# Optimization experiments

Hardware: AMD Instinct MI355X
Metric: run time of the kernel (lower is better)

## Reference

```python
import jax, jax.numpy as jnp
import numpy as np

N_EMBD = 1024  # C in forward; scale is C**-0.5 (full embed dim, per source)


def setup_inputs() -> dict:
    key = jax.random.key(0)
    k1, k2, k3, k4 = jax.random.split(key, 4)
    B, T, C, H = 4, 4096, N_EMBD, 64
    x = jax.random.normal(k1, (B, T, C), dtype=jnp.float32)
    # weights stored as [in, out] = [n_embd, head_size]
    Wq = jax.random.normal(k2, (C, H), dtype=jnp.float32) * (C ** -0.5)
    Wk = jax.random.normal(k3, (C, H), dtype=jnp.float32) * (C ** -0.5)
    Wv = jax.random.normal(k4, (C, H), dtype=jnp.float32) * (C ** -0.5)
    return {"x": x, "Wq": Wq, "Wk": Wk, "Wv": Wv}


def reference(x, Wq, Wk, Wv):
    # x: [B, T, C]; projections to head_size H
    C = x.shape[-1]
    q = jnp.einsum('btc,ch->bth', x, Wq)  # [B,T,H]
    k = jnp.einsum('btc,ch->bth', x, Wk)  # [B,T,H]
    v = jnp.einsum('btc,ch->bth', x, Wv)  # [B,T,H]
    # scores scaled by C**-0.5 (full embed dim, matching original module)
    wei = jnp.einsum('bth,bsh->bts', q, k) * (C ** -0.5)  # [B,T,T]
    wei = jax.nn.softmax(wei, axis=-1)  # dropout p=0 -> identity
    out = jnp.einsum('bts,bsh->bth', wei, v)  # [B,T,H]
    return out
```

## Files before the change

kernel.cpp:

```cpp
#include <hip/hip_runtime.h>
#include <hip/hip_bf16.h>


#define BB 4
#define TT 4096
#define CC 1024
#define HH 64

typedef __attribute__((ext_vector_type(8))) short bf16x8;
typedef __attribute__((ext_vector_type(4))) float f32x4;

#if __has_builtin(__builtin_amdgcn_exp2f)
#define EXP2(x) __builtin_amdgcn_exp2f(x)
#else
#define EXP2(x) exp2f(x)
#endif

__device__ __forceinline__ short f2bf(float f) {
  union { float f; unsigned u; } v; v.f = f;
  unsigned r = v.u + 0x7fffu + ((v.u >> 16) & 1u);
  return (short)(r >> 16);
}

__device__ __forceinline__ unsigned pk2bf(float lo, float hi) {
  __hip_bfloat162 p = __float22bfloat162_rn(make_float2(lo, hi));
  return *reinterpret_cast<unsigned*>(&p);
}

__device__ __forceinline__ void gload16(const void* g, short* l) {
  __builtin_amdgcn_global_load_lds(
      (const __attribute__((address_space(1))) void*)g,
      (__attribute__((address_space(3))) void*)l, 16, 0, 0);
}

#define WAITVM0() asm volatile("s_waitcnt vmcnt(0)" ::: "memory")

__global__ void wtf_kernel(const float* __restrict__ Wq, const float* __restrict__ Wk,
                           const float* __restrict__ Wv, short* __restrict__ WtF) {
  int idx = blockIdx.x * 256 + threadIdx.x;
  int lane = idx & 63, ks = (idx >> 6) & 31, nf = idx >> 11;
  int l15 = lane & 15, lg = lane >> 4;
  int n = nf * 16 + l15;
  const float* W = (n < HH) ? Wq : ((n < 2 * HH) ? Wk : Wv);
  float sc = (n < HH) ? (0.03125f * 1.44269504f) : 1.0f;
  int k0 = ks * 32 + lg * 8, h = n & (HH - 1);
  bf16x8 r;
#pragma unroll
  for (int j = 0; j < 8; ++j) r[j] = f2bf(W[(k0 + j) * HH + h] * sc);
  *(bf16x8*)(WtF + (size_t)idx * 8) = r;
}

__launch_bounds__(256, 2)
__global__ void projX_kernel(const float* __restrict__ x, const short* __restrict__ WtF,
                             short* __restrict__ qo, short* __restrict__ kFo,
                             short* __restrict__ vFo) {
  __shared__ __align__(16) short xs[32768];
  int t = threadIdx.x;
  int row0 = blockIdx.x * 16;
  int wave = t >> 6, lane = t & 63;
  int l15 = lane & 15, lg = lane >> 4;

  {
    const float* xb = x + (size_t)row0 * CC;
    int lp = lane ^ (lane >> 3);
#pragma unroll
    for (int k2 = 0; k2 < 16; ++k2) {
      int ks = wave * 8 + (k2 >> 1);
      int ln = (k2 & 1) * 32 + (lp >> 1);
      int h  = lp & 1;
      const float* src = xb + (size_t)(ln & 15) * CC + ks * 32 + (ln >> 4) * 8 + h * 4;
      short* dst = xs + ((size_t)wave * 1024 + (size_t)k2 * 64) * 8;
      gload16(src, dst);
    }
  }

  int nf0 = wave * 3;
  const short* wp = WtF + ((size_t)nf0 * 32 * 64 + (size_t)lane) * 8;

  f32x4 acc[3];
#pragma unroll
  for (int j = 0; j < 3; ++j) acc[j] = (f32x4){0.f, 0.f, 0.f, 0.f};

  WAITVM0();
  __syncthreads();

  const char* xsb = (const char*)xs;
  int m = (lane >> 2) & 7;
  int roA = ((lane * 2) ^ m) * 16;
  int roB = ((lane * 2 + 1) ^ m) * 16;

#define LDA(KS, AV)                                                  \
  {                                                                  \
    float4 fa_ = *(const float4*)(xsb + (KS) * 2048 + roA);          \
    float4 fb_ = *(const float4*)(xsb + (KS) * 2048 + roB);          \
    unsigned* au_ = (unsigned*)&(AV);                                \
    au_[0] = pk2bf(fa_.x, fa_.y); au_[1] = pk2bf(fa_.z, fa_.w);      \
    au_[2] = pk2bf(fb_.x, fb_.y); au_[3] = pk2bf(fb_.z, fb_.w);      \
  }

  bf16x8 wA[3], wB[3];
#pragma unroll
  for (int j = 0; j < 3; ++j) wA[j] = *(const bf16x8*)(wp + (size_t)j * 32 * 512);

#pragma unroll
  for (int ks = 0; ks < 32; ks += 2) {
#pragma unroll
    for (int j = 0; j < 3; ++j)
      wB[j] = *(const bf16x8*)(wp + ((size_t)j * 32 + ks + 1) * 512);
    bf16x8 a0;
    LDA(ks, a0)
#pragma unroll
    for (int j = 0; j < 3; ++j)
      acc[j] = __builtin_amdgcn_mfma_f32_16x16x32_bf16(a0, wA[j], acc[j], 0, 0, 0);
    if (ks + 2 < 32) {
#pragma unroll
      for (int j = 0; j < 3; ++j)
        wA[j] = *(const bf16x8*)(wp + ((size_t)j * 32 + ks + 2) * 512);
    }
    bf16x8 a1;
    LDA(ks + 1, a1)
#pragma unroll
    for (int j = 0; j < 3; ++j)
      acc[j] = __builtin_amdgcn_mfma_f32_16x16x32_bf16(a1, wB[j], acc[j], 0, 0, 0);
  }
#undef LDA

  int b  = row0 >> 12;
  int kt = (row0 & 4095) >> 6;
  int cf = (row0 >> 4) & 3;
  short* ksl = xs;
  short* vsl = xs + 1152;

  __syncthreads();

#pragma unroll
  for (int j = 0; j < 3; ++j) {
    int nf = nf0 + j;
    int h = (nf & 3) * 16 + l15;
    if (nf < 4) {
#pragma unroll
      for (int reg = 0; reg < 4; ++reg)
        qo[(size_t)(row0 + lg * 4 + reg) * HH + h] = f2bf(acc[j][reg]);
    } else if (nf < 8) {
#pragma unroll
      for (int reg = 0; reg < 4; ++reg)
        ksl[(lg * 4 + reg) * 72 + h] = f2bf(acc[j][reg]);
    } else {
      uint2 w2;
      w2.x = pk2bf(acc[j][0], acc[j][1]);
      w2.y = pk2bf(acc[j][2], acc[j][3]);
      *(uint2*)(vsl + h * 24 + lg * 4) = w2;
    }
  }
  __syncthreads();

  size_t tileoff = ((size_t)b * 64 + kt) * 4096;
  if (t < 128) {
    int ks2 = t >> 6, ln = t & 63;
    int l15o = ln & 15, lgo = ln >> 4;
    bf16x8 r = *(const bf16x8*)(ksl + l15o * 72 + ks2 * 32 + lgo * 8);
    *(bf16x8*)(kFo + tileoff + (size_t)(cf * 2 + ks2) * 512 + ln * 8) = r;
  } else if (t < 256) {
    int t2 = t - 128;
    int hf = t2 >> 5, lgl = (t2 >> 4) & 1, l15o = t2 & 15;
    bf16x8 r = *(const bf16x8*)(vsl + (hf * 16 + l15o) * 24 + lgl * 8);
    int lnout = (2 * (cf & 1) + lgl) * 16 + l15o;
    *(bf16x8*)(vFo + tileoff + (size_t)(hf * 2 + (cf >> 1)) * 512 + lnout * 8) = r;
  }
}

__launch_bounds__(512, 4)
__global__ void attnW_kernel(const short* __restrict__ q, const short* __restrict__ kF,
                             const short* __restrict__ vF, float* __restrict__ out) {
  __shared__ __align__(16) short ps[8][2560];
  __shared__ __align__(16) float macc[32][68];
  __shared__ float lL[32];
  int wave = threadIdx.x >> 6, lane = threadIdx.x & 63;
  int l15 = lane & 15, lg = lane >> 4;
  int low3 = blockIdx.x & 7;
  int b  = low3 >> 1;
  int qt = ((blockIdx.x >> 3) << 1) | (low3 & 1);
  int brow0 = qt * 32;

  const short* qb = q + ((size_t)b * TT + brow0 + l15) * HH;
  bf16x8 qa[2][2];
#pragma unroll
  for (int g = 0; g < 2; ++g) {
    qa[g][0] = *(const bf16x8*)(qb + g * 16 * HH + lg * 8);
    qa[g][1] = *(const bf16x8*)(qb + g * 16 * HH + 32 + lg * 8);
  }

  bf16x8 ones;
#pragma unroll
  for (int j = 0; j < 8; ++j) ones[j] = (short)0x3F80;

  const short* kfb = kF + (size_t)b * 262144 + (size_t)lane * 8;
  const short* vfb = vF + (size_t)b * 262144 + (size_t)lane * 8;

  f32x4 acc[2][4], accl[2];
#pragma unroll
  for (int g = 0; g < 2; ++g) {
#pragma unroll
    for (int i = 0; i < 4; ++i) acc[g][i] = (f32x4){0.f, 0.f, 0.f, 0.f};
    accl[g] = (f32x4){0.f, 0.f, 0.f, 0.f};
  }

  char* psw = (char*)&ps[wave][0];
  int xorv = (l15 >> 3) << 4;
  int pwbase = l15 * 80;
  int pr = l15 * 80 + ((lg << 4) ^ xorv);

  for (int t = wave * 16; t < wave * 16 + 16; ++t) {
    const short* kp = kfb + (size_t)t * 2048;
    const short* vp = vfb + (size_t)(t >> 1) * 4096 + (size_t)(t & 1) * 512;
    bf16x8 kf[4], vf[4];
#pragma unroll
    for (int ld = 0; ld < 4; ++ld) kf[ld] = *(const bf16x8*)(kp + ld * 512);
#pragma unroll
    for (int hf = 0; hf < 4; ++hf) vf[hf] = *(const bf16x8*)(vp + hf * 1024);
#pragma unroll
    for (int g = 0; g < 2; ++g)
#pragma unroll
      for (int cf = 0; cf < 2; ++cf) {
        f32x4 t4 = (f32x4){0.f, 0.f, 0.f, 0.f};
        t4 = __builtin_amdgcn_mfma_f32_16x16x32_bf16(kf[cf * 2], qa[g][0], t4, 0, 0, 0);
        t4 = __builtin_amdgcn_mfma_f32_16x16x32_bf16(kf[cf * 2 + 1], qa[g][1], t4, 0, 0, 0);
        float p0 = EXP2(t4[0]), p1 = EXP2(t4[1]);
        float p2 = EXP2(t4[2]), p3 = EXP2(t4[3]);
        unsigned w01 = pk2bf(p0, p1);
        unsigned w23 = pk2bf(p2, p3);
        int cb = (cf << 5) + (lg << 3);
        *(unsigned*)(psw + g * 1280 + pwbase + ((cb) ^ xorv)) = w01;
        *(unsigned*)(psw + g * 1280 + pwbase + ((cb + 4) ^ xorv)) = w23;
      }
    bf16x8 pa0 = *(const bf16x8*)(psw + pr);
    bf16x8 pa1 = *(const bf16x8*)(psw + 1280 + pr);
    __builtin_amdgcn_s_setprio(1);
#pragma unroll
    for (int hf = 0; hf < 4; ++hf) {
      acc[0][hf] = __builtin_amdgcn_mfma_f32_16x16x32_bf16(pa0, vf[hf], acc[0][hf], 0, 0, 0);
      acc[1][hf] = __builtin_amdgcn_mfma_f32_16x16x32_bf16(pa1, vf[hf], acc[1][hf], 0, 0, 0);
    }
    accl[0] = __builtin_amdgcn_mfma_f32_16x16x32_bf16(pa0, ones, accl[0], 0, 0, 0);
    accl[1] = __builtin_amdgcn_mfma_f32_16x16x32_bf16(pa1, ones, accl[1], 0, 0, 0);
    __builtin_amdgcn_s_setprio(0);
  }

#pragma unroll
  for (int ph = 0; ph < 8; ++ph) {
    if (wave == ph) {
#pragma unroll
      for (int g = 0; g < 2; ++g)
#pragma unroll
        for (int reg = 0; reg < 4; ++reg) {
          int row = g * 16 + lg * 4 + reg;
          if (ph == 0) {
#pragma unroll
            for (int hf = 0; hf < 4; ++hf)
              macc[row][hf * 16 + l15] = acc[g][hf][reg];
            if (l15 == 0) lL[row] = accl[g][reg];
          } else {
#pragma unroll
            for (int hf = 0; hf < 4; ++hf)
              macc[row][hf * 16 + l15] += acc[g][hf][reg];
            if (l15 == 0) lL[row] += accl[g][reg];
          }
        }
    }
    __syncthreads();
  }

  {
    int tt = threadIdx.x;
    int r = tt >> 4, c0 = (tt & 15) * 4;
    float linv = 1.0f / lL[r];
    float4 o;
    o.x = macc[r][c0 + 0] * linv; o.y = macc[r][c0 + 1] * linv;
    o.z = macc[r][c0 + 2] * linv; o.w = macc[r][c0 + 3] * linv;
    *(float4*)(out + ((size_t)b * TT + brow0 + r) * HH + c0) = o;
  }
}

extern "C" void kernel_launch(void* const* d_in, const int* in_sizes, int n_in,
                              void* d_out, int out_size, void* d_ws, size_t ws_size,
                              hipStream_t stream) {
  const float* x  = (const float*)d_in[0];
  const float* Wq = (const float*)d_in[1];
  const float* Wk = (const float*)d_in[2];
  const float* Wv = (const float*)d_in[3];
  float* out = (float*)d_out;

  char* ws = (char*)d_ws;
  short* WtF = (short*)ws;
  short* q   = (short*)(ws + 0x080000);
  short* kF  = (short*)(ws + 0x280000);
  short* vF  = (short*)(ws + 0x480000);

  hipLaunchKernelGGL(wtf_kernel,   dim3(96),   dim3(256), 0, stream, Wq, Wk, Wv, WtF);
  hipLaunchKernelGGL(projX_kernel, dim3(1024), dim3(256), 0, stream, x, WtF, q, kF, vF);
  hipLaunchKernelGGL(attnW_kernel, dim3(512),  dim3(512), 0, stream, q, kF, vF, out);
}
```

Measured before the change: 65.16 us.

## Split projection K dimension across waves with shared-memory reduction

After: 67.97 us. 1.04x slower.

```diff
diff --git a/kernel.cpp b/kernel.cpp
--- a/kernel.cpp
+++ b/kernel.cpp
@@ -50,36 +50,37 @@
   *(bf16x8*)(WtF + (size_t)idx * 8) = r;
 }
 
-__launch_bounds__(256, 2)
-__global__ void projX_kernel(const float* __restrict__ x, const short* __restrict__ WtF,
+__launch_bounds__(512, 4)
+__global__ void projK_kernel(const float* __restrict__ x, const short* __restrict__ WtF,
                              short* __restrict__ qo, short* __restrict__ kFo,
                              short* __restrict__ vFo) {
   __shared__ __align__(16) short xs[32768];
+  __shared__ float macc[16][200];
   int t = threadIdx.x;
   int row0 = blockIdx.x * 16;
   int wave = t >> 6, lane = t & 63;
   int l15 = lane & 15, lg = lane >> 4;
+  int ng = wave & 1, kg = wave >> 1;
 
   {
     const float* xb = x + (size_t)row0 * CC;
     int lp = lane ^ (lane >> 3);
 #pragma unroll
-    for (int k2 = 0; k2 < 16; ++k2) {
-      int ks = wave * 8 + (k2 >> 1);
+    for (int k2 = 0; k2 < 8; ++k2) {
+      int ks = wave * 4 + (k2 >> 1);
       int ln = (k2 & 1) * 32 + (lp >> 1);
       int h  = lp & 1;
       const float* src = xb + (size_t)(ln & 15) * CC + ks * 32 + (ln >> 4) * 8 + h * 4;
-      short* dst = xs + ((size_t)wave * 1024 + (size_t)k2 * 64) * 8;
+      short* dst = xs + ((size_t)wave * 512 + (size_t)k2 * 64) * 8;
       gload16(src, dst);
     }
   }
 
-  int nf0 = wave * 3;
-  const short* wp = WtF + ((size_t)nf0 * 32 * 64 + (size_t)lane) * 8;
-
-  f32x4 acc[3];
-#pragma unroll
-  for (int j = 0; j < 3; ++j) acc[j] = (f32x4){0.f, 0.f, 0.f, 0.f};
+  const short* wp = WtF + ((size_t)(ng * 6) * 32 * 64 + (size_t)lane) * 8;
+
+  f32x4 acc[6];
+#pragma unroll
+  for (int j = 0; j < 6; ++j) acc[j] = (f32x4){0.f, 0.f, 0.f, 0.f};
 
   WAITVM0();
   __syncthreads();
@@ -98,58 +99,85 @@
     au_[2] = pk2bf(fb_.x, fb_.y); au_[3] = pk2bf(fb_.z, fb_.w);      \
   }
 
-  bf16x8 wA[3], wB[3];
-#pragma unroll
-  for (int j = 0; j < 3; ++j) wA[j] = *(const bf16x8*)(wp + (size_t)j * 32 * 512);
-
-#pragma unroll
-  for (int ks = 0; ks < 32; ks += 2) {
-#pragma unroll
-    for (int j = 0; j < 3; ++j)
+  bf16x8 wA[6], wB[6];
+  int ks0 = kg * 8;
+#pragma unroll
+  for (int j = 0; j < 6; ++j)
+    wA[j] = *(const bf16x8*)(wp + ((size_t)j * 32 + ks0) * 512);
+
+#pragma unroll
+  for (int ksl = 0; ksl < 8; ksl += 2) {
+    int ks = ks0 + ksl;
+#pragma unroll
+    for (int j = 0; j < 6; ++j)
       wB[j] = *(const bf16x8*)(wp + ((size_t)j * 32 + ks + 1) * 512);
     bf16x8 a0;
     LDA(ks, a0)
 #pragma unroll
-    for (int j = 0; j < 3; ++j)
+    for (int j = 0; j < 6; ++j)
       acc[j] = __builtin_amdgcn_mfma_f32_16x16x32_bf16(a0, wA[j], acc[j], 0, 0, 0);
-    if (ks + 2 < 32) {
-#pragma unroll
-      for (int j = 0; j < 3; ++j)
+    if (ksl + 2 < 8) {
+#pragma unroll
+      for (int j = 0; j < 6; ++j)
         wA[j] = *(const bf16x8*)(wp + ((size_t)j * 32 + ks + 2) * 512);
     }
     bf16x8 a1;
     LDA(ks + 1, a1)
 #pragma unroll
-    for (int j = 0; j < 3; ++j)
+    for (int j = 0; j < 6; ++j)
       acc[j] = __builtin_amdgcn_mfma_f32_16x16x32_bf16(a1, wB[j], acc[j], 0, 0, 0);
   }
 #undef LDA
+
+#pragma unroll
+  for (int p = 0; p < 4; ++p) {
+    if (kg == p) {
+#pragma unroll
+      for (int j = 0; j < 6; ++j) {
+        int col = (ng * 6 + j) * 16 + l15;
+#pragma unroll
+        for (int reg = 0; reg < 4; ++reg) {
+          int row = lg * 4 + reg;
+          if (p == 0) macc[row][col] = acc[j][reg];
+          else        macc[row][col] += acc[j][reg];
+        }
+      }
+    }
+    __syncthreads();
+  }
 
   int b  = row0 >> 12;
   int kt = (row0 & 4095) >> 6;
   int cf = (row0 >> 4) & 3;
-  short* ksl = xs;
-  short* vsl = xs + 1152;
-
-  __syncthreads();
-
-#pragma unroll
-  for (int j = 0; j < 3; ++j) {
-    int nf = nf0 + j;
-    int h = (nf & 3) * 16 + l15;
-    if (nf < 4) {
-#pragma unroll
-      for (int reg = 0; reg < 4; ++reg)
-        qo[(size_t)(row0 + lg * 4 + reg) * HH + h] = f2bf(acc[j][reg]);
-    } else if (nf < 8) {
-#pragma unroll
-      for (int reg = 0; reg < 4; ++reg)
-        ksl[(lg * 4 + reg) * 72 + h] = f2bf(acc[j][reg]);
-    } else {
-      uint2 w2;
-      w2.x = pk2bf(acc[j][0], acc[j][1]);
-      w2.y = pk2bf(acc[j][2], acc[j][3]);
-      *(uint2*)(vsl + h * 24 + lg * 4) = w2;
+  short* kstg = xs;
+  short* vstg = xs + 1152;
+
+  if (t < 256) {
+    int epw = wave;
+#pragma unroll
+    for (int j = 0; j < 3; ++j) {
+      int nf = epw * 3 + j;
+      int h = (nf & 3) * 16 + l15;
+      float v0 = macc[lg * 4 + 0][nf * 16 + l15];
+      float v1 = macc[lg * 4 + 1][nf * 16 + l15];
+      float v2 = macc[lg * 4 + 2][nf * 16 + l15];
+      float v3 = macc[lg * 4 + 3][nf * 16 + l15];
+      if (nf < 4) {
+        qo[(size_t)(row0 + lg * 4 + 0) * HH + h] = f2bf(v0);
+        qo[(size_t)(row0 + lg * 4 + 1) * HH + h] = f2bf(v1);
+        qo[(size_t)(row0 + lg * 4 + 2) * HH + h] = f2bf(v2);
+        qo[(size_t)(row0 + lg * 4 + 3) * HH + h] = f2bf(v3);
+      } else if (nf < 8) {
+        kstg[(lg * 4 + 0) * 72 + h] = f2bf(v0);
+        kstg[(lg * 4 + 1) * 72 + h] = f2bf(v1);
+        kstg[(lg * 4 + 2) * 72 + h] = f2bf(v2);
+        kstg[(lg * 4 + 3) * 72 + h] = f2bf(v3);
+      } else {
+        uint2 w2;
+        w2.x = pk2bf(v0, v1);
+        w2.y = pk2bf(v2, v3);
+        *(uint2*)(vstg + h * 24 + lg * 4) = w2;
+      }
     }
   }
   __syncthreads();
@@ -158,12 +186,12 @@
   if (t < 128) {
     int ks2 = t >> 6, ln = t & 63;
     int l15o = ln & 15, lgo = ln >> 4;
-    bf16x8 r = *(const bf16x8*)(ksl + l15o * 72 + ks2 * 32 + lgo * 8);
+    bf16x8 r = *(const bf16x8*)(kstg + l15o * 72 + ks2 * 32 + lgo * 8);
     *(bf16x8*)(kFo + tileoff + (size_t)(cf * 2 + ks2) * 512 + ln * 8) = r;
   } else if (t < 256) {
     int t2 = t - 128;
     int hf = t2 >> 5, lgl = (t2 >> 4) & 1, l15o = t2 & 15;
-    bf16x8 r = *(const bf16x8*)(vsl + (hf * 16 + l15o) * 24 + lgl * 8);
+    bf16x8 r = *(const bf16x8*)(vstg + (hf * 16 + l15o) * 24 + lgl * 8);
     int lnout = (2 * (cf & 1) + lgl) * 16 + l15o;
     *(bf16x8*)(vFo + tileoff + (size_t)(hf * 2 + (cf >> 1)) * 512 + lnout * 8) = r;
   }
@@ -297,6 +325,6 @@
   short* vF  = (short*)(ws + 0x480000);
 
   hipLaunchKernelGGL(wtf_kernel,   dim3(96),   dim3(256), 0, stream, Wq, Wk, Wv, WtF);
-  hipLaunchKernelGGL(projX_kernel, dim3(1024), dim3(256), 0, stream, x, WtF, q, kF, vF);
+  hipLaunchKernelGGL(projK_kernel, dim3(1024), dim3(512), 0, stream, x, WtF, q, kF, vF);
   hipLaunchKernelGGL(attnW_kernel, dim3(512),  dim3(512), 0, stream, q, kF, vF, out);
 }
```
